# Optimization experiments

Measured on AMD Instinct MI355X. Metric: run time of the kernel, lower is better.

## Reference

```python
import jax, jax.numpy as jnp
import numpy as np

B, T, C, H, DI = 4, 1024, 1024, 16, 128
TAU = 1.0
LAMBDA_CONF = 0.1
SYS2_THR = 1.0


def _ln(x, w, b):
    mu = x.mean(-1, keepdims=True)
    var = x.var(-1, keepdims=True)
    return (x - mu) * jax.lax.rsqrt(var + 1e-5) * w + b


def setup_inputs() -> dict:
    key = jax.random.key(0)
    ks = jax.random.split(key, 16)
    s = lambda i, shape: jax.random.normal(ks[i], shape, jnp.float32) * 0.02
    return {
        "h": jax.random.normal(ks[0], (B, T, C), jnp.float32),
        "ln_w": jnp.ones((C,), jnp.float32), "ln_b": jnp.zeros((C,), jnp.float32),
        "w_q": s(1, (C, C)), "w_k": s(2, (C, C)), "w_v": s(3, (C, C)),
        "w_o": s(4, (C, C)), "b_o": jnp.zeros((C,), jnp.float32),
        "U": s(5, (C, DI)), "V": s(6, (DI, C)),
        "gamma_w": s(7, (C, 1)), "gamma_b": jnp.zeros((1,), jnp.float32),
        "mass_w": s(8, (C, 1)), "mass_b": jnp.zeros((1,), jnp.float32),
        "eps_w": s(9, (C, 1)), "eps_b": jnp.zeros((1,), jnp.float32),
        "lg_w1": s(10, (C, 4 * C)), "lg_b1": jnp.zeros((4 * C,), jnp.float32),
        "lg_w2": s(11, (4 * C, C)), "lg_b2": jnp.zeros((C,), jnp.float32),
        "mlp_w1": s(12, (C, 4 * C)), "mlp_b1": jnp.zeros((4 * C,), jnp.float32),
        "mlp_w2": s(13, (4 * C, C)), "mlp_b2": jnp.zeros((C,), jnp.float32),
    }


def reference(h, ln_w, ln_b, w_q, w_k, w_v, w_o, b_o, U, V,
              gamma_w, gamma_b, mass_w, mass_b, eps_w, eps_b,
              lg_w1, lg_b1, lg_w2, lg_b2, mlp_w1, mlp_b1, mlp_w2, mlp_b2):
    hd = C // H
    h_norm = _ln(h, ln_w, ln_b)

    # ---- HamiltonianAttention (conservative force field) ----
    q = (h_norm @ w_q).reshape(B, T, H, hd).transpose(0, 2, 1, 3)  # [B,H,T,hd]
    k = (h_norm @ w_k).reshape(B, T, H, hd).transpose(0, 2, 1, 3)
    v = (h_norm @ w_v).reshape(B, T, H, hd).transpose(0, 2, 1, 3)
    scores = jnp.einsum('bhqd,bhkd->bhqk', q, k) / (hd ** 0.5) / TAU
    attn = jax.nn.softmax(scores, axis=-1)
    force = jnp.einsum('bhqk,bhkd->bhqd', attn, v).transpose(0, 2, 1, 3).reshape(B, T, C)
    f_attn = force @ w_o + b_o

    # ---- total force, low-rank projection ----
    f_total = f_attn - LAMBDA_CONF * h_norm
    f_proj = f_total @ U                               # [B,T,DI]

    # ---- FSI (force stability index) ----
    h_mag = jnp.linalg.norm(h_norm, axis=-1)           # [B,T]
    f_mag = jnp.linalg.norm(f_proj, axis=-1)
    fsi = h_mag / (2.0 * f_mag + 1e-6)

    # ---- CognitiveGearbox: per-token mass / timestep ----
    mass = 1.0 + jax.nn.softplus(h @ mass_w + mass_b)  # [B,T,1], mass >= 1
    eps = jax.nn.sigmoid(h @ eps_w + eps_b)            # [B,T,1], eps in (0,1)
    gamma = jax.nn.sigmoid(h_norm @ gamma_w + gamma_b) # [B,T,1] damping gate

    # ---- fused AGI momentum recurrence: m_t = gamma_t*m_{t-1} + (eps_t/mass_t)*f_t ----
    def step(m, inps):
        f_t, g_t, e_t, ms_t = inps                     # [B,DI],[B,1],[B,1],[B,1]
        m = g_t * m + (e_t / ms_t) * f_t
        return m, m

    xs = (f_proj.transpose(1, 0, 2), gamma.transpose(1, 0, 2),
          eps.transpose(1, 0, 2), mass.transpose(1, 0, 2))
    m0 = jnp.zeros((B, DI), h.dtype)
    _, m_seq = jax.lax.scan(step, m0, xs)              # [T,B,DI]
    m_new = m_seq.transpose(1, 0, 2)                   # [B,T,DI]

    # ---- position update + system-2 correction + MLP ----
    velocity = m_new @ V                               # [B,T,C]
    h_new = h + eps * velocity
    hn2 = _ln(h_new, ln_w, ln_b)
    sys2 = jax.nn.gelu(hn2 @ lg_w1 + lg_b1, approximate=False) @ lg_w2 + lg_b2
    gate = jax.nn.sigmoid(mass - SYS2_THR)
    h_final = h_new + gate * sys2
    hn3 = _ln(h_final, ln_w, ln_b)
    h_final = h_final + (jax.nn.gelu(hn3 @ mlp_w1 + mlp_b1, approximate=False) @ mlp_w2 + mlp_b2)
    return (h_final, m_new, fsi)
```

## Files before the change

kernel.cpp:

```cpp
#include <hip/hip_runtime.h>
#include <hip/hip_bf16.h>
#include <math.h>

typedef __attribute__((ext_vector_type(8))) short bf16x8;
typedef __attribute__((ext_vector_type(4))) float f32x4;

#define DEVI __device__ __forceinline__

constexpr int B_ = 4, T_ = 1024, C_ = 1024, H_ = 16, HD_ = 64, DI_ = 128;
constexpr int NTOK = B_ * T_;
constexpr int C4 = 4 * C_;
constexpr int C3 = 3 * C_;
constexpr float LAMBDA_CONF = 0.1f;

DEVI short f2bf(float f) {
  unsigned u = __builtin_bit_cast(unsigned, f);
  u += 0x7fffu + ((u >> 16) & 1u);
  return (short)(u >> 16);
}
DEVI unsigned pk2(float a, float b) {
  return (unsigned)(unsigned short)f2bf(a) | ((unsigned)(unsigned short)f2bf(b) << 16);
}
DEVI float sigm(float x) { return 1.f / (1.f + __expf(-x)); }
DEVI float geluf(float x) { return 0.5f * x * (1.f + erff(x * 0.70710678118654752440f)); }

DEVI void gload16(const void* g, void* l) {
  __builtin_amdgcn_global_load_lds((const __attribute__((address_space(1))) unsigned*)g,
                                   (__attribute__((address_space(3))) unsigned*)l, 16, 0, 0);
}

template <int EPI>
DEVI void epi_store(void* Outp, const float* bias, const float* resid, const float* tokv,
                    int row, int col, int N, float v) {
  size_t idx = (size_t)row * N + col;
  if (EPI == 0) {
    ((float*)Outp)[idx] = v;
  } else if (EPI == 1) {
    ((short*)Outp)[idx] = f2bf(v);
  } else if (EPI == 2) {
    ((short*)Outp)[idx] = f2bf(v + bias[col] - LAMBDA_CONF * resid[idx]);
  } else if (EPI == 3) {
    ((float*)Outp)[idx] = resid[idx] + tokv[row] * v;
  } else if (EPI == 4) {
    float x = v + bias[col];
    ((short*)Outp)[idx] = f2bf(geluf(x));
  } else if (EPI == 5) {
    float x = v + bias[col];
    float g = sigm(tokv[row] - 1.f);
    ((float*)Outp)[idx] = resid[idx] + g * x;
  } else if (EPI == 6) {
    ((float*)Outp)[idx] = resid[idx] + v + bias[col];
  }
}

__global__ __launch_bounds__(256) void transpose_cvt(const float* __restrict__ W,
                                                     short* __restrict__ Wt, int K, int N) {
  __shared__ float s[32][33];
  int n0 = blockIdx.x * 32, k0 = blockIdx.y * 32;
  int tx = threadIdx.x & 31, ty = threadIdx.x >> 5;
#pragma unroll
  for (int i = 0; i < 4; i++)
    s[ty + i * 8][tx] = W[(size_t)(k0 + ty + i * 8) * N + n0 + tx];
  __syncthreads();
#pragma unroll
  for (int i = 0; i < 4; i++)
    Wt[(size_t)(n0 + ty + i * 8) * K + k0 + tx] = f2bf(s[tx][ty + i * 8]);
}

__global__ __launch_bounds__(256) void transpose_v(const short* __restrict__ QKV,
                                                   short* __restrict__ VT) {
  __shared__ short s[32][33];
  int bh = blockIdx.z;
  int b = bh >> 4, h = bh & 15;
  int t0 = blockIdx.x * 32, d0 = blockIdx.y * 32;
  int tx = threadIdx.x & 31, ty = threadIdx.x >> 5;
#pragma unroll
  for (int i = 0; i < 4; i++)
    s[ty + i * 8][tx] =
        QKV[(size_t)(b * T_ + t0 + ty + i * 8) * C3 + 2 * C_ + h * 64 + d0 + tx];
  __syncthreads();
#pragma unroll
  for (int i = 0; i < 4; i++)
    VT[((size_t)bh * 64 + d0 + ty + i * 8) * T_ + t0 + tx] = s[tx][ty + i * 8];
}

DEVI float blk_red(float v, volatile float* sm) {
  int lane = threadIdx.x & 63, wv = threadIdx.x >> 6;
#pragma unroll
  for (int o = 32; o; o >>= 1) v += __shfl_down(v, o);
  __syncthreads();
  if (lane == 0) sm[wv] = v;
  __syncthreads();
  return sm[0] + sm[1] + sm[2] + sm[3];
}

template <int FULL, int WF32>
__global__ __launch_bounds__(256) void ln_kernel(
    const float* __restrict__ X, const float* __restrict__ lnw, const float* __restrict__ lnb,
    float* __restrict__ Out, short* __restrict__ OutBf,
    const float* __restrict__ gw, const float* __restrict__ gb,
    const float* __restrict__ mw, const float* __restrict__ mb,
    const float* __restrict__ ew, const float* __restrict__ eb,
    float* __restrict__ gammaA, float* __restrict__ epsA, float* __restrict__ massA,
    float* __restrict__ coefA, float* __restrict__ hmagA) {
  __shared__ float sm[4];
  int tok = blockIdx.x;
  const float* x = X + (size_t)tok * C_;
  int t4 = threadIdx.x * 4;
  float4 xv = *(const float4*)&x[t4];
  float s = xv.x + xv.y + xv.z + xv.w;
  float ss = xv.x * xv.x + xv.y * xv.y + xv.z * xv.z + xv.w * xv.w;
  s = blk_red(s, sm);
  ss = blk_red(ss, sm);
  float mu = s * (1.f / C_);
  float var = ss * (1.f / C_) - mu * mu;
  float rs = rsqrtf(var + 1e-5f);
  float4 wv = *(const float4*)&lnw[t4];
  float4 bv = *(const float4*)&lnb[t4];
  float4 hn;
  hn.x = (xv.x - mu) * rs * wv.x + bv.x;
  hn.y = (xv.y - mu) * rs * wv.y + bv.y;
  hn.z = (xv.z - mu) * rs * wv.z + bv.z;
  hn.w = (xv.w - mu) * rs * wv.w + bv.w;
  if (WF32) *(float4*)&Out[(size_t)tok * C_ + t4] = hn;
  short4 ob;
  ob.x = f2bf(hn.x); ob.y = f2bf(hn.y); ob.z = f2bf(hn.z); ob.w = f2bf(hn.w);
  *(short4*)&OutBf[(size_t)tok * C_ + t4] = ob;
  if (FULL) {
    float4 gwv = *(const float4*)&gw[t4];
    float4 mwv = *(const float4*)&mw[t4];
    float4 ewv = *(const float4*)&ew[t4];
    float gd = hn.x * gwv.x + hn.y * gwv.y + hn.z * gwv.z + hn.w * gwv.w;
    float md = xv.x * mwv.x + xv.y * mwv.y + xv.z * mwv.z + xv.w * mwv.w;
    float ed = xv.x * ewv.x + xv.y * ewv.y + xv.z * ewv.z + xv.w * ewv.w;
    float h2 = hn.x * hn.x + hn.y * hn.y + hn.z * hn.z + hn.w * hn.w;
    gd = blk_red(gd, sm);
    md = blk_red(md, sm);
    ed = blk_red(ed, sm);
    h2 = blk_red(h2, sm);
    if (threadIdx.x == 0) {
      float g = sigm(gd + gb[0]);
      float xm = md + mb[0];
      float sp = (xm > 20.f) ? xm : log1pf(expf(xm));
      float msv = 1.f + sp;
      float epv = sigm(ed + eb[0]);
      gammaA[tok] = g;
      massA[tok] = msv;
      epsA[tok] = epv;
      coefA[tok] = epv / msv;
      hmagA[tok] = sqrtf(h2);
    }
  }
}

template <int EPI, int NB, int BNFAST>
__global__ __launch_bounds__(256, 3) void gemmS(
    const short* __restrict__ A, const short* __restrict__ Bt, void* __restrict__ Outp,
    const float* __restrict__ bias, const float* __restrict__ resid,
    const float* __restrict__ tokv, int M, int N, int K) {
  constexpr int NFR = NB / 32;
  __shared__ short As[128][32];
  __shared__ short Bs[NB][32];
  int tid = threadIdx.x, lane = tid & 63, w = tid >> 6;
  int wr = w >> 1, wc = w & 1;
  int fr = lane & 15, fg = lane >> 4;
  int xm = (fr >> 1) & 3;
  int cpx = gridDim.x >> 3;
  int bid = (blockIdx.x & 7) * cpx + (blockIdx.x >> 3);
  int bm, bn;
  if constexpr (BNFAST) {
    int nN = N / NB;
    bn = (bid % nN) * NB;
    bm = (bid / nN) << 7;
  } else {
    int nM = M >> 7;
    bm = (bid % nM) << 7;
    bn = (bid / nM) * NB;
  }
  f32x4 acc[4][NFR] = {};

  int jsw = (lane & 3) ^ ((lane >> 3) & 3);
  const short* gA = A + (size_t)(bm + w * 32 + (lane >> 2)) * K + (jsw << 3);
  const short* gB;
  if constexpr (NB == 128)
    gB = Bt + (size_t)(bn + w * 32 + (lane >> 2)) * K + (jsw << 3);
  else
    gB = Bt + (size_t)(bn + w * 16 + (lane >> 2)) * K + (jsw << 3);

  for (int kt = 0; kt < K; kt += 32) {
    gload16(gA + kt, &As[w * 32][0]);
    gload16(gA + (size_t)16 * K + kt, &As[w * 32 + 16][0]);
    if constexpr (NB == 128) {
      gload16(gB + kt, &Bs[w * 32][0]);
      gload16(gB + (size_t)16 * K + kt, &Bs[w * 32 + 16][0]);
    } else {
      gload16(gB + kt, &Bs[w * 16][0]);
    }
    __syncthreads();
    bf16x8 af[4], bv[NFR];
#pragma unroll
    for (int i = 0; i < 4; i++)
      af[i] = *(const bf16x8*)&As[wr * 64 + i * 16 + fr][(fg ^ xm) << 3];
#pragma unroll
    for (int j = 0; j < NFR; j++)
      bv[j] = *(const bf16x8*)&Bs[wc * (NB / 2) + j * 16 + fr][(fg ^ xm) << 3];
#pragma unroll
    for (int mi = 0; mi < 4; mi++)
#pragma unroll
      for (int ni = 0; ni < NFR; ni++)
        acc[mi][ni] = __builtin_amdgcn_mfma_f32_16x16x32_bf16(af[mi], bv[ni], acc[mi][ni], 0, 0, 0);
    __syncthreads();
  }

#pragma unroll
  for (int mi = 0; mi < 4; mi++) {
    int row0 = bm + wr * 64 + mi * 16 + fg * 4;
#pragma unroll
    for (int ni = 0; ni < NFR; ni++) {
      int col = bn + wc * (NB / 2) + ni * 16 + fr;
#pragma unroll
      for (int r = 0; r < 4; r++)
        epi_store<EPI>(Outp, bias, resid, tokv, row0 + r, col, N, acc[mi][ni][r]);
    }
  }
}

template <int EPI>
__global__ __launch_bounds__(256) void gemm128(
    const short* __restrict__ A, const short* __restrict__ Bt, void* __restrict__ Outp,
    const float* __restrict__ bias, const float* __restrict__ resid,
    const float* __restrict__ tokv, int M, int N, int K) {
  __shared__ short As[3][128][32];
  __shared__ short Bs[3][128][32];
  int tid = threadIdx.x, lane = tid & 63, w = tid >> 6;
  int wr = w >> 1, wc = w & 1;
  int fr = lane & 15, fg = lane >> 4;
  int xm = (fr >> 1) & 3;
  int nM = M >> 7;
  int cpx = gridDim.x >> 3;
  int bid = (blockIdx.x & 7) * cpx + (blockIdx.x >> 3);
  int bm = (bid % nM) << 7;
  int bn = (bid / nM) << 7;
  f32x4 acc[4][4] = {};

  int jsw = (lane & 3) ^ ((lane >> 3) & 3);
  const short* gA = A + (size_t)(bm + w * 32 + (lane >> 2)) * K + (jsw << 3);
  const short* gB = Bt + (size_t)(bn + w * 32 + (lane >> 2)) * K + (jsw << 3);

  auto stage = [&](int buf, int kt) {
#pragma unroll
    for (int g = 0; g < 2; g++) {
      gload16(gA + (size_t)(g * 16) * K + kt, &As[buf][w * 32 + g * 16][0]);
      gload16(gB + (size_t)(g * 16) * K + kt, &Bs[buf][w * 32 + g * 16][0]);
    }
  };

  int nt = K >> 5;
  stage(0, 0);
  if (nt > 1) stage(1, 32);
  for (int t = 0; t < nt; t++) {
    if (t + 1 < nt) asm volatile("s_waitcnt vmcnt(4)" ::: "memory");
    else asm volatile("s_waitcnt vmcnt(0)" ::: "memory");
    __builtin_amdgcn_s_barrier();
    __builtin_amdgcn_sched_barrier(0);
    int nb = t + 2;
    if (nb < nt) stage(nb % 3, nb << 5);
    int cb = t % 3;
    bf16x8 af[4], bfv[4];
#pragma unroll
    for (int i = 0; i < 4; i++)
      af[i] = *(const bf16x8*)&As[cb][wr * 64 + i * 16 + fr][(fg ^ xm) << 3];
#pragma unroll
    for (int i = 0; i < 4; i++)
      bfv[i] = *(const bf16x8*)&Bs[cb][wc * 64 + i * 16 + fr][(fg ^ xm) << 3];
#pragma unroll
    for (int mi = 0; mi < 4; mi++)
#pragma unroll
      for (int ni = 0; ni < 4; ni++)
        acc[mi][ni] = __builtin_amdgcn_mfma_f32_16x16x32_bf16(af[mi], bfv[ni], acc[mi][ni], 0, 0, 0);
    __builtin_amdgcn_sched_barrier(0);
    __builtin_amdgcn_s_barrier();
  }

#pragma unroll
  for (int mi = 0; mi < 4; mi++) {
    int row0 = bm + wr * 64 + mi * 16 + fg * 4;
#pragma unroll
    for (int ni = 0; ni < 4; ni++) {
      int col = bn + wc * 64 + ni * 16 + fr;
#pragma unroll
      for (int r = 0; r < 4; r++)
        epi_store<EPI>(Outp, bias, resid, tokv, row0 + r, col, N, acc[mi][ni][r]);
    }
  }
}

__global__ __launch_bounds__(256) void attn_kernel(const short* __restrict__ QKV,
                                                   const short* __restrict__ VT,
                                                   short* __restrict__ Fout) {
  __shared__ short Ks[2][64][64];
  __shared__ short Vts[2][64][64];
  __shared__ short Ps[4][16][72];
  int bh = blockIdx.y;
  int b = bh >> 4, h = bh & 15;
  int qt0 = blockIdx.x * 64;
  int tid = threadIdx.x, lane = tid & 63, w = tid >> 6;
  int fr = lane & 15, fg = lane >> 4;

  size_t base = ((size_t)b * T_) * C3 + h * 64;
  const short* Qp = QKV + base;
  const short* Kp = QKV + base + C_;
  const short* Vtp = VT + (size_t)bh * 64 * T_;
  int qrow = qt0 + w * 16 + fr;
  bf16x8 qf0 = *(const bf16x8*)&Qp[(size_t)qrow * C3 + fg * 8];
  bf16x8 qf1 = *(const bf16x8*)&Qp[(size_t)qrow * C3 + 32 + fg * 8];

  f32x4 oacc[4] = {};
  float m_run = -1e30f, l_run = 0.f;

  int jsw = (lane & 7) ^ ((lane >> 3) & 7);
  int sr8 = w * 8;
  int rsub = lane >> 3;

  auto stage = [&](int buf, int kt) {
#pragma unroll
    for (int c = 0; c < 2; c++) {
      int row = c * 32 + sr8 + rsub;
      gload16(Kp + (size_t)(kt + row) * C3 + jsw * 8, &Ks[buf][c * 32 + sr8][0]);
      gload16(Vtp + (size_t)row * T_ + kt + jsw * 8, &Vts[buf][c * 32 + sr8][0]);
    }
  };

  stage(0, 0);
  for (int t = 0; t < T_ / 64; t++) {
    if (t + 1 < T_ / 64) {
      stage((t + 1) & 1, (t + 1) * 64);
      asm volatile("s_waitcnt vmcnt(4)" ::: "memory");
    } else {
      asm volatile("s_waitcnt vmcnt(0)" ::: "memory");
    }
    __builtin_amdgcn_s_barrier();
    __builtin_amdgcn_sched_barrier(0);
    int cb = t & 1;

    f32x4 sacc[4];
#pragma unroll
    for (int kb = 0; kb < 4; kb++) {
      bf16x8 k0 = *(const bf16x8*)&Ks[cb][kb * 16 + fr][(fg ^ (fr & 7)) << 3];
      bf16x8 k1 = *(const bf16x8*)&Ks[cb][kb * 16 + fr][((4 | fg) ^ (fr & 7)) << 3];
      f32x4 z = {};
      z = __builtin_amdgcn_mfma_f32_16x16x32_bf16(k0, qf0, z, 0, 0, 0);
      z = __builtin_amdgcn_mfma_f32_16x16x32_bf16(k1, qf1, z, 0, 0, 0);
      sacc[kb] = z;
    }
    float mt = -1e30f;
#pragma unroll
    for (int kb = 0; kb < 4; kb++)
#pragma unroll
      for (int r = 0; r < 4; r++) {
        sacc[kb][r] *= 0.125f;
        mt = fmaxf(mt, sacc[kb][r]);
      }
    mt = fmaxf(mt, __shfl_xor(mt, 16));
    mt = fmaxf(mt, __shfl_xor(mt, 32));
    float m_new = fmaxf(m_run, mt);
    float alpha = __expf(m_run - m_new);
    float psum = 0.f;
    float pv[16];
#pragma unroll
    for (int kb = 0; kb < 4; kb++)
#pragma unroll
      for (int r = 0; r < 4; r++) {
        float p = __expf(sacc[kb][r] - m_new);
        pv[kb * 4 + r] = p;
        psum += p;
      }
    psum += __shfl_xor(psum, 16);
    psum += __shfl_xor(psum, 32);
    l_run = l_run * alpha + psum;
    m_run = m_new;

#pragma unroll
    for (int kb = 0; kb < 4; kb++) {
      uint2 pp;
      pp.x = pk2(pv[kb * 4 + 0], pv[kb * 4 + 1]);
      pp.y = pk2(pv[kb * 4 + 2], pv[kb * 4 + 3]);
      *(uint2*)&Ps[w][fr][kb * 16 + fg * 4] = pp;
    }
    float ar[4];
#pragma unroll
    for (int r = 0; r < 4; r++) ar[r] = __shfl(alpha, fg * 4 + r);
#pragma unroll
    for (int ni = 0; ni < 4; ni++)
#pragma unroll
      for (int r = 0; r < 4; r++) oacc[ni][r] *= ar[r];

    asm volatile("s_waitcnt lgkmcnt(0)" ::: "memory");
    __builtin_amdgcn_sched_barrier(0);
    bf16x8 pa0 = *(const bf16x8*)&Ps[w][fr][fg * 8];
    bf16x8 pa1 = *(const bf16x8*)&Ps[w][fr][32 + fg * 8];
#pragma unroll
    for (int ni = 0; ni < 4; ni++) {
      bf16x8 v0 = *(const bf16x8*)&Vts[cb][ni * 16 + fr][(fg ^ (fr & 7)) << 3];
      bf16x8 v1 = *(const bf16x8*)&Vts[cb][ni * 16 + fr][((4 | fg) ^ (fr & 7)) << 3];
      oacc[ni] = __builtin_amdgcn_mfma_f32_16x16x32_bf16(pa0, v0, oacc[ni], 0, 0, 0);
      oacc[ni] = __builtin_amdgcn_mfma_f32_16x16x32_bf16(pa1, v1, oacc[ni], 0, 0, 0);
    }
    __builtin_amdgcn_sched_barrier(0);
    __builtin_amdgcn_s_barrier();
  }

  float lr4[4];
#pragma unroll
  for (int r = 0; r < 4; r++) lr4[r] = __shfl(l_run, fg * 4 + r);
#pragma unroll
  for (int ni = 0; ni < 4; ni++)
#pragma unroll
    for (int r = 0; r < 4; r++) {
      int tok = b * T_ + qt0 + w * 16 + fg * 4 + r;
      Fout[(size_t)tok * C_ + h * 64 + ni * 16 + fr] = f2bf(oacc[ni][r] / lr4[r]);
    }
}

__global__ __launch_bounds__(128) void scan_kernel(const float* __restrict__ f_proj,
                                                   const float* __restrict__ gam,
                                                   const float* __restrict__ coef,
                                                   float* __restrict__ m_out,
                                                   short* __restrict__ m_bf) {
  int b = blockIdx.x;
  int d = threadIdx.x;
  const float* fp = f_proj + (size_t)b * T_ * DI_ + d;
  const float* g = gam + (size_t)b * T_;
  const float* c = coef + (size_t)b * T_;
  float* mo = m_out + (size_t)b * T_ * DI_ + d;
  short* mb = m_bf + (size_t)b * T_ * DI_ + d;
  float m = 0.f;
  for (int t = 0; t < T_; t += 8) {
    float fv[8], gv[8], cv[8];
#pragma unroll
    for (int i = 0; i < 8; i++) {
      fv[i] = fp[(size_t)(t + i) * DI_];
      gv[i] = g[t + i];
      cv[i] = c[t + i];
    }
#pragma unroll
    for (int i = 0; i < 8; i++) {
      m = gv[i] * m + cv[i] * fv[i];
      mo[(size_t)(t + i) * DI_] = m;
      mb[(size_t)(t + i) * DI_] = f2bf(m);
    }
  }
}

__global__ __launch_bounds__(256) void fsi_kernel(const float* __restrict__ f_proj,
                                                  const float* __restrict__ hmag,
                                                  float* __restrict__ fsi_out) {
  int tok = blockIdx.x * 4 + (threadIdx.x >> 6);
  int l = threadIdx.x & 63;
  float2 v = *(const float2*)&f_proj[(size_t)tok * DI_ + l * 2];
  float s = v.x * v.x + v.y * v.y;
#pragma unroll
  for (int o = 32; o; o >>= 1) s += __shfl_down(s, o);
  if (l == 0) fsi_out[tok] = hmag[tok] / (2.f * sqrtf(s) + 1e-6f);
}

extern "C" void kernel_launch(void* const* d_in, const int* in_sizes, int n_in,
                              void* d_out, int out_size, void* d_ws, size_t ws_size,
                              hipStream_t stream) {
  (void)in_sizes; (void)n_in; (void)out_size; (void)ws_size;
  const float* h = (const float*)d_in[0];
  const float* ln_w = (const float*)d_in[1];
  const float* ln_b = (const float*)d_in[2];
  const float* w_q = (const float*)d_in[3];
  const float* w_k = (const float*)d_in[4];
  const float* w_v = (const float*)d_in[5];
  const float* w_o = (const float*)d_in[6];
  const float* b_o = (const float*)d_in[7];
  const float* U = (const float*)d_in[8];
  const float* V = (const float*)d_in[9];
  const float* gamma_w = (const float*)d_in[10];
  const float* gamma_b = (const float*)d_in[11];
  const float* mass_w = (const float*)d_in[12];
  const float* mass_b = (const float*)d_in[13];
  const float* eps_w = (const float*)d_in[14];
  const float* eps_b = (const float*)d_in[15];
  const float* lg_w1 = (const float*)d_in[16];
  const float* lg_b1 = (const float*)d_in[17];
  const float* lg_w2 = (const float*)d_in[18];
  const float* lg_b2 = (const float*)d_in[19];
  const float* mlp_w1 = (const float*)d_in[20];
  const float* mlp_b1 = (const float*)d_in[21];
  const float* mlp_w2 = (const float*)d_in[22];
  const float* mlp_b2 = (const float*)d_in[23];

  float* out_h = (float*)d_out;
  float* out_m = out_h + (size_t)NTOK * C_;
  float* out_fsi = out_m + (size_t)NTOK * DI_;

  char* wsb = (char*)d_ws;
  size_t off = 0;
  auto al = [&](size_t bytes) {
    void* p = wsb + off;
    off += (bytes + 255) & ~(size_t)255;
    return p;
  };
  short* wqkvt = (short*)al((size_t)C3 * C_ * 2);
  short* wot = (short*)al((size_t)C_ * C_ * 2);
  short* ut = (short*)al((size_t)DI_ * C_ * 2);
  short* vt = (short*)al((size_t)C_ * DI_ * 2);
  short* lg1t = (short*)al((size_t)C4 * C_ * 2);
  short* lg2t = (short*)al((size_t)C_ * C4 * 2);
  short* mlp1t = (short*)al((size_t)C4 * C_ * 2);
  short* mlp2t = (short*)al((size_t)C_ * C4 * 2);
  float* h_norm = (float*)al((size_t)NTOK * C_ * 4);
  short* hn_bf = (short*)al((size_t)NTOK * C_ * 2);
  short* qkv_bf = (short*)al((size_t)NTOK * C3 * 2);
  short* tmp_bf = (short*)al((size_t)NTOK * C_ * 2);
  float* f_proj = (float*)al((size_t)NTOK * DI_ * 4);
  short* act = (short*)al((size_t)NTOK * C4 * 2);
  float* h_pre = (float*)al((size_t)NTOK * C_ * 4);
  short* vtrans = (short*)al((size_t)B_ * H_ * 64 * T_ * 2);
  float* gammaA = (float*)al((size_t)NTOK * 4);
  float* epsA = (float*)al((size_t)NTOK * 4);
  float* massA = (float*)al((size_t)NTOK * 4);
  float* coefA = (float*)al((size_t)NTOK * 4);
  float* hmagA = (float*)al((size_t)NTOK * 4);
  short* ftot_bf = hn_bf;
  short* m_bf = act;
  float* h_new = (float*)qkv_bf;

  dim3 blk(256);
  transpose_cvt<<<dim3(C_ / 32, C_ / 32), blk, 0, stream>>>(w_q, wqkvt, C_, C_);
  transpose_cvt<<<dim3(C_ / 32, C_ / 32), blk, 0, stream>>>(w_k, wqkvt + (size_t)C_ * C_, C_, C_);
  transpose_cvt<<<dim3(C_ / 32, C_ / 32), blk, 0, stream>>>(w_v, wqkvt + (size_t)2 * C_ * C_, C_, C_);
  transpose_cvt<<<dim3(C_ / 32, C_ / 32), blk, 0, stream>>>(w_o, wot, C_, C_);
  transpose_cvt<<<dim3(DI_ / 32, C_ / 32), blk, 0, stream>>>(U, ut, C_, DI_);
  transpose_cvt<<<dim3(C_ / 32, DI_ / 32), blk, 0, stream>>>(V, vt, DI_, C_);
  transpose_cvt<<<dim3(C4 / 32, C_ / 32), blk, 0, stream>>>(lg_w1, lg1t, C_, C4);
  transpose_cvt<<<dim3(C_ / 32, C4 / 32), blk, 0, stream>>>(lg_w2, lg2t, C4, C_);
  transpose_cvt<<<dim3(C4 / 32, C_ / 32), blk, 0, stream>>>(mlp_w1, mlp1t, C_, C4);
  transpose_cvt<<<dim3(C_ / 32, C4 / 32), blk, 0, stream>>>(mlp_w2, mlp2t, C4, C_);

  ln_kernel<1, 1><<<NTOK, blk, 0, stream>>>(h, ln_w, ln_b, h_norm, hn_bf, gamma_w, gamma_b,
                                            mass_w, mass_b, eps_w, eps_b, gammaA, epsA, massA,
                                            coefA, hmagA);
  gemmS<1, 128, 0><<<(NTOK / 128) * (C3 / 128), blk, 0, stream>>>(hn_bf, wqkvt, qkv_bf, nullptr,
                                                                  nullptr, nullptr, NTOK, C3, C_);
  transpose_v<<<dim3(T_ / 32, 2, B_ * H_), blk, 0, stream>>>(qkv_bf, vtrans);
  attn_kernel<<<dim3(T_ / 64, B_ * H_), blk, 0, stream>>>(qkv_bf, vtrans, tmp_bf);
  gemmS<2, 64, 1><<<(NTOK / 128) * (C_ / 64), blk, 0, stream>>>(tmp_bf, wot, ftot_bf, b_o,
                                                                h_norm, nullptr, NTOK, C_, C_);
  gemm128<0><<<(NTOK / 128) * (DI_ / 128), blk, 0, stream>>>(ftot_bf, ut, f_proj, nullptr,
                                                             nullptr, nullptr, NTOK, DI_, C_);
  fsi_kernel<<<NTOK / 4, blk, 0, stream>>>(f_proj, hmagA, out_fsi);
  scan_kernel<<<B_, dim3(DI_), 0, stream>>>(f_proj, gammaA, coefA, out_m, m_bf);
  gemmS<3, 64, 0><<<(NTOK / 128) * (C_ / 64), blk, 0, stream>>>(m_bf, vt, h_new, nullptr, h,
                                                                epsA, NTOK, C_, DI_);
  ln_kernel<0, 0><<<NTOK, blk, 0, stream>>>(h_new, ln_w, ln_b, nullptr, tmp_bf, nullptr, nullptr,
                                            nullptr, nullptr, nullptr, nullptr, nullptr, nullptr,
                                            nullptr, nullptr, nullptr);
  gemmS<4, 128, 0><<<(NTOK / 128) * (C4 / 128), blk, 0, stream>>>(tmp_bf, lg1t, act, lg_b1,
                                                                  nullptr, nullptr, NTOK, C4, C_);
  gemmS<5, 64, 1><<<(NTOK / 128) * (C_ / 64), blk, 0, stream>>>(act, lg2t, h_pre, lg_b2,
                                                                h_new, massA, NTOK, C_, C4);
  ln_kernel<0, 0><<<NTOK, blk, 0, stream>>>(h_pre, ln_w, ln_b, nullptr, tmp_bf, nullptr, nullptr,
                                            nullptr, nullptr, nullptr, nullptr, nullptr, nullptr,
                                            nullptr, nullptr, nullptr);
  gemmS<4, 128, 0><<<(NTOK / 128) * (C4 / 128), blk, 0, stream>>>(tmp_bf, mlp1t, act, mlp_b1,
                                                                  nullptr, nullptr, NTOK, C4, C_);
  gemmS<6, 64, 1><<<(NTOK / 128) * (C_ / 64), blk, 0, stream>>>(act, mlp2t, out_h, mlp_b2,
                                                                h_pre, nullptr, NTOK, C_, C4);
}
```

Baseline: 523.8 us.

## Replace N=C output GEMMs with 64x64-tile single-buffered kernel

```diff
diff --git a/kernel.cpp b/kernel.cpp
--- a/kernel.cpp
+++ b/kernel.cpp
@@ -154,7 +154,7 @@
 }
 
 template <int EPI, int NB, int BNFAST>
-__global__ __launch_bounds__(256, 3) void gemmS(
+__global__ __launch_bounds__(256, 4) void gemmS(
     const short* __restrict__ A, const short* __restrict__ Bt, void* __restrict__ Outp,
     const float* __restrict__ bias, const float* __restrict__ resid,
     const float* __restrict__ tokv, int M, int N, int K) {
@@ -226,68 +226,52 @@
 }
 
 template <int EPI>
-__global__ __launch_bounds__(256) void gemm128(
+__global__ __launch_bounds__(256, 4) void gemmS64(
     const short* __restrict__ A, const short* __restrict__ Bt, void* __restrict__ Outp,
     const float* __restrict__ bias, const float* __restrict__ resid,
     const float* __restrict__ tokv, int M, int N, int K) {
-  __shared__ short As[3][128][32];
-  __shared__ short Bs[3][128][32];
+  __shared__ short As[64][32];
+  __shared__ short Bs[64][32];
   int tid = threadIdx.x, lane = tid & 63, w = tid >> 6;
   int wr = w >> 1, wc = w & 1;
   int fr = lane & 15, fg = lane >> 4;
   int xm = (fr >> 1) & 3;
-  int nM = M >> 7;
   int cpx = gridDim.x >> 3;
   int bid = (blockIdx.x & 7) * cpx + (blockIdx.x >> 3);
-  int bm = (bid % nM) << 7;
-  int bn = (bid / nM) << 7;
-  f32x4 acc[4][4] = {};
+  int nN = N >> 6;
+  int bn = (bid % nN) << 6;
+  int bm = (bid / nN) << 6;
+  f32x4 acc[2][2] = {};
 
   int jsw = (lane & 3) ^ ((lane >> 3) & 3);
-  const short* gA = A + (size_t)(bm + w * 32 + (lane >> 2)) * K + (jsw << 3);
-  const short* gB = Bt + (size_t)(bn + w * 32 + (lane >> 2)) * K + (jsw << 3);
-
-  auto stage = [&](int buf, int kt) {
-#pragma unroll
-    for (int g = 0; g < 2; g++) {
-      gload16(gA + (size_t)(g * 16) * K + kt, &As[buf][w * 32 + g * 16][0]);
-      gload16(gB + (size_t)(g * 16) * K + kt, &Bs[buf][w * 32 + g * 16][0]);
-    }
-  };
-
-  int nt = K >> 5;
-  stage(0, 0);
-  if (nt > 1) stage(1, 32);
-  for (int t = 0; t < nt; t++) {
-    if (t + 1 < nt) asm volatile("s_waitcnt vmcnt(4)" ::: "memory");
-    else asm volatile("s_waitcnt vmcnt(0)" ::: "memory");
-    __builtin_amdgcn_s_barrier();
-    __builtin_amdgcn_sched_barrier(0);
-    int nb = t + 2;
-    if (nb < nt) stage(nb % 3, nb << 5);
-    int cb = t % 3;
-    bf16x8 af[4], bfv[4];
-#pragma unroll
-    for (int i = 0; i < 4; i++)
-      af[i] = *(const bf16x8*)&As[cb][wr * 64 + i * 16 + fr][(fg ^ xm) << 3];
-#pragma unroll
-    for (int i = 0; i < 4; i++)
-      bfv[i] = *(const bf16x8*)&Bs[cb][wc * 64 + i * 16 + fr][(fg ^ xm) << 3];
-#pragma unroll
-    for (int mi = 0; mi < 4; mi++)
-#pragma unroll
-      for (int ni = 0; ni < 4; ni++)
-        acc[mi][ni] = __builtin_amdgcn_mfma_f32_16x16x32_bf16(af[mi], bfv[ni], acc[mi][ni], 0, 0, 0);
-    __builtin_amdgcn_sched_barrier(0);
-    __builtin_amdgcn_s_barrier();
-  }
-
-#pragma unroll
-  for (int mi = 0; mi < 4; mi++) {
-    int row0 = bm + wr * 64 + mi * 16 + fg * 4;
-#pragma unroll
-    for (int ni = 0; ni < 4; ni++) {
-      int col = bn + wc * 64 + ni * 16 + fr;
+  const short* gA = A + (size_t)(bm + w * 16 + (lane >> 2)) * K + (jsw << 3);
+  const short* gB = Bt + (size_t)(bn + w * 16 + (lane >> 2)) * K + (jsw << 3);
+
+  for (int kt = 0; kt < K; kt += 32) {
+    gload16(gA + kt, &As[w * 16][0]);
+    gload16(gB + kt, &Bs[w * 16][0]);
+    __syncthreads();
+    bf16x8 af[2], bv[2];
+#pragma unroll
+    for (int i = 0; i < 2; i++)
+      af[i] = *(const bf16x8*)&As[wr * 32 + i * 16 + fr][(fg ^ xm) << 3];
+#pragma unroll
+    for (int j = 0; j < 2; j++)
+      bv[j] = *(const bf16x8*)&Bs[wc * 32 + j * 16 + fr][(fg ^ xm) << 3];
+#pragma unroll
+    for (int mi = 0; mi < 2; mi++)
+#pragma unroll
+      for (int ni = 0; ni < 2; ni++)
+        acc[mi][ni] = __builtin_amdgcn_mfma_f32_16x16x32_bf16(af[mi], bv[ni], acc[mi][ni], 0, 0, 0);
+    __syncthreads();
+  }
+
+#pragma unroll
+  for (int mi = 0; mi < 2; mi++) {
+    int row0 = bm + wr * 32 + mi * 16 + fg * 4;
+#pragma unroll
+    for (int ni = 0; ni < 2; ni++) {
+      int col = bn + wc * 32 + ni * 16 + fr;
 #pragma unroll
       for (int r = 0; r < 4; r++)
         epi_store<EPI>(Outp, bias, resid, tokv, row0 + r, col, N, acc[mi][ni][r]);
@@ -548,26 +532,26 @@
                                                                   nullptr, nullptr, NTOK, C3, C_);
   transpose_v<<<dim3(T_ / 32, 2, B_ * H_), blk, 0, stream>>>(qkv_bf, vtrans);
   attn_kernel<<<dim3(T_ / 64, B_ * H_), blk, 0, stream>>>(qkv_bf, vtrans, tmp_bf);
-  gemmS<2, 64, 1><<<(NTOK / 128) * (C_ / 64), blk, 0, stream>>>(tmp_bf, wot, ftot_bf, b_o,
-                                                                h_norm, nullptr, NTOK, C_, C_);
-  gemm128<0><<<(NTOK / 128) * (DI_ / 128), blk, 0, stream>>>(ftot_bf, ut, f_proj, nullptr,
-                                                             nullptr, nullptr, NTOK, DI_, C_);
+  gemmS64<2><<<(NTOK / 64) * (C_ / 64), blk, 0, stream>>>(tmp_bf, wot, ftot_bf, b_o,
+                                                          h_norm, nullptr, NTOK, C_, C_);
+  gemmS64<0><<<(NTOK / 64) * (DI_ / 64), blk, 0, stream>>>(ftot_bf, ut, f_proj, nullptr,
+                                                           nullptr, nullptr, NTOK, DI_, C_);
   fsi_kernel<<<NTOK / 4, blk, 0, stream>>>(f_proj, hmagA, out_fsi);
   scan_kernel<<<B_, dim3(DI_), 0, stream>>>(f_proj, gammaA, coefA, out_m, m_bf);
-  gemmS<3, 64, 0><<<(NTOK / 128) * (C_ / 64), blk, 0, stream>>>(m_bf, vt, h_new, nullptr, h,
-                                                                epsA, NTOK, C_, DI_);
+  gemmS64<3><<<(NTOK / 64) * (C_ / 64), blk, 0, stream>>>(m_bf, vt, h_new, nullptr, h,
+                                                          epsA, NTOK, C_, DI_);
   ln_kernel<0, 0><<<NTOK, blk, 0, stream>>>(h_new, ln_w, ln_b, nullptr, tmp_bf, nullptr, nullptr,
                                             nullptr, nullptr, nullptr, nullptr, nullptr, nullptr,
                                             nullptr, nullptr, nullptr);
   gemmS<4, 128, 0><<<(NTOK / 128) * (C4 / 128), blk, 0, stream>>>(tmp_bf, lg1t, act, lg_b1,
                                                                   nullptr, nullptr, NTOK, C4, C_);
-  gemmS<5, 64, 1><<<(NTOK / 128) * (C_ / 64), blk, 0, stream>>>(act, lg2t, h_pre, lg_b2,
-                                                                h_new, massA, NTOK, C_, C4);
+  gemmS64<5><<<(NTOK / 64) * (C_ / 64), blk, 0, stream>>>(act, lg2t, h_pre, lg_b2,
+                                                          h_new, massA, NTOK, C_, C4);
   ln_kernel<0, 0><<<NTOK, blk, 0, stream>>>(h_pre, ln_w, ln_b, nullptr, tmp_bf, nullptr, nullptr,
                                             nullptr, nullptr, nullptr, nullptr, nullptr, nullptr,
                                             nullptr, nullptr, nullptr);
   gemmS<4, 128, 0><<<(NTOK / 128) * (C4 / 128), blk, 0, stream>>>(tmp_bf, mlp1t, act, mlp_b1,
                                                                   nullptr, nullptr, NTOK, C4, C_);
-  gemmS<6, 64, 1><<<(NTOK / 128) * (C_ / 64), blk, 0, stream>>>(act, mlp2t, out_h, mlp_b2,
-                                                                h_pre, nullptr, NTOK, C_, C4);
-}
+  gemmS64<6><<<(NTOK / 64) * (C_ / 64), blk, 0, stream>>>(act, mlp2t, out_h, mlp_b2,
+                                                          h_pre, nullptr, NTOK, C_, C4);
+}
```

Result: faster. 478.7 us (-8.6%).
